# Kernel tuning notes

Measured on AMD Instinct MI355X. Metric: run time of the kernel, lower is better.

Reference implementation:

```python
import jax, jax.numpy as jnp
from jax import lax
import numpy as np

K = 1024      # kernel_size
S = 256       # stride
CUT = 513     # kernel_size//2 + 1
TC = 2 * CUT  # transform_channels = 1026
CH = 8        # combine_hidden
B = 32
TIME = 262144


def setup_inputs() -> dict:
    key = jax.random.key(0)
    ks = jax.random.split(key, 12)
    x = jax.random.normal(ks[0], (B, 1, TIME), dtype=jnp.float32)
    conv1_w = jax.random.normal(ks[1], (TC, 1, K), dtype=jnp.float32) * 0.02
    in_gamma = 1.0 + 0.1 * jax.random.normal(ks[2], (TC,), dtype=jnp.float32)
    comb1_w = jax.random.normal(ks[3], (CH, 2), dtype=jnp.float32) * 0.5
    comb1_b = jax.random.normal(ks[4], (CH,), dtype=jnp.float32) * 0.1
    comb2_w = jax.random.normal(ks[5], (1, CH), dtype=jnp.float32) * 0.5
    comb2_b = jax.random.normal(ks[6], (1,), dtype=jnp.float32) * 0.1
    lin_w = jax.random.normal(ks[7], (CUT, CUT), dtype=jnp.float32) * 0.04
    lin_b = jax.random.normal(ks[8], (CUT,), dtype=jnp.float32) * 0.02
    fc_gamma = 1.0 + 0.1 * jax.random.normal(ks[9], (CUT,), dtype=jnp.float32)
    convT_w = jax.random.normal(ks[10], (TC, 2, K), dtype=jnp.float32) * 0.02  # torch ConvTranspose1d (Cin, Cout, K)
    return {"x": x, "conv1_w": conv1_w, "in_gamma": in_gamma,
            "comb1_w": comb1_w, "comb1_b": comb1_b,
            "comb2_w": comb2_w, "comb2_b": comb2_b,
            "lin_w": lin_w, "lin_b": lin_b, "fc_gamma": fc_gamma,
            "convT_w": convT_w}


def reference(x, conv1_w, in_gamma, comb1_w, comb1_b, comb2_w, comb2_b,
              lin_w, lin_b, fc_gamma, convT_w):
    time = x.shape[2]
    # conv1: Conv1d(1, TC, K, stride=S, padding=K), no bias
    t = lax.conv_general_dilated(x, conv1_w, window_strides=(S,),
                                 padding=[(K, K)],
                                 dimension_numbers=("NCH", "OIH", "NCH"))
    # ConvScaler1d (per-channel scale) + tanh activation
    t = jnp.tanh(t * in_gamma[None, :, None])  # (B, TC, F)
    real_x, imag_x = t[:, :CUT, :], t[:, CUT:, :]
    spec = jnp.stack([real_x, imag_x], axis=1)  # (B, 2, CUT, F)
    # combine1/combine2: 1x1 Conv2d + relu
    h = jax.nn.relu(jnp.einsum("bcxf,oc->boxf", spec, comb1_w)
                    + comb1_b[None, :, None, None])
    h = jax.nn.relu(jnp.einsum("bcxf,oc->boxf", h, comb2_w)
                    + comb2_b[None, :, None, None])[:, 0]  # (B, CUT, F)
    # FC over frequency axis per (batch, frame)
    hh = h.transpose(0, 2, 1)  # (B, F, CUT)
    hh = (hh @ lin_w.T + lin_b) * fc_gamma  # BitwiseLinear + Scaler
    mask = (jnp.tanh(hh) + 1.0) * 0.5       # output_transform -> [0,1]
    mask = mask.transpose(0, 2, 1)          # (B, CUT, F)
    mask = jnp.concatenate([mask, mask], axis=1)  # (B, TC, F)
    t = t * mask
    # conv1_transpose: ConvTranspose1d(TC, 2, K, stride=S), no bias
    wt = jnp.flip(convT_w.transpose(1, 0, 2), axis=2)  # (2, TC, K) flipped
    y = lax.conv_general_dilated(t, wt, window_strides=(1,),
                                 padding=[(K - 1, K - 1)],
                                 lhs_dilation=(S,),
                                 dimension_numbers=("NCH", "OIH", "NCH"))
    y = y[:, :, K:time + K]  # (B, 2, time)
    return jax.nn.softmax(y, axis=1)
```

## Files before the change

### kernel.cpp

```cpp
#include <hip/hip_runtime.h>
#include <cstddef>
#include <cstdint>

#define TIME_N 262144
#define BATCH  32
#define KW     1024
#define ST     256
#define CUTN   513
#define TCN    1026
#define FN     1029
#define FPAD   1152
#define CPAD   1152
#define XLEN   (FPAD * ST + KW)
#define XBLK   (XLEN / 256)

#define MROWS  (BATCH * FN)
#define MP     33024
#define KPH    544
#define NPH    640
#define TBP    1040
#define FLATB  (FN * TBP)
#define KPC    4160

#define PB_XPAD  (XBLK * BATCH)
#define PB_WBF   (PB_XPAD + CPAD)
#define PB_WLIN  (PB_WBF + NPH)
#define PB_TOTAL (PB_WLIN + KPC)

typedef __bf16 bf16x8 __attribute__((ext_vector_type(8)));
typedef float floatx4 __attribute__((ext_vector_type(4)));

__device__ __forceinline__ unsigned short f2bf(float f) {
    union { float f; unsigned u; } v; v.f = f;
    unsigned r = (v.u + 0x7fffu + ((v.u >> 16) & 1u)) >> 16;
    return (unsigned short)r;
}
__device__ __forceinline__ float bf2f(unsigned short s) {
    union { unsigned u; float f; } v; v.u = ((unsigned)s) << 16;
    return v.f;
}
__device__ __forceinline__ int permch(int n) {
    return (n & 1) ? (CUTN + (n >> 1)) : (n >> 1);
}

__device__ __forceinline__ void load_lds16(const void* g, void* l) {
    __builtin_amdgcn_global_load_lds(
        (const __attribute__((address_space(1))) void*)g,
        (__attribute__((address_space(3))) void*)l, 16, 0, 0);
}

__global__ __launch_bounds__(256) void k_prep(
    const float* __restrict__ x, const float* __restrict__ c1w,
    const float* __restrict__ lw, const float* __restrict__ wct,
    unsigned short* __restrict__ xb, unsigned short* __restrict__ wbf,
    unsigned short* __restrict__ wlb, unsigned short* __restrict__ wdb)
{
    const int bid = blockIdx.x;
    if (bid < PB_XPAD) {
        const int b = bid / XBLK;
        const int p = (bid - b * XBLK) * 256 + threadIdx.x;
        const int g = p - KW;
        float v = (g >= 0 && g < TIME_N) ? x[(size_t)b * TIME_N + g] : 0.0f;
        xb[(size_t)b * XLEN + p] = f2bf(v);
    } else if (bid < PB_WBF) {
        const int n = bid - PB_XPAD;
        const int ch = (n < TCN) ? permch(n) : 0;
        for (int k = threadIdx.x; k < KW; k += 256) {
            float v = (n < TCN) ? c1w[(size_t)ch * KW + k] : 0.0f;
            wbf[(size_t)n * KW + k] = f2bf(v);
        }
    } else if (bid < PB_WLIN) {
        const int n = bid - PB_WBF;
        for (int k = threadIdx.x; k < KPH; k += 256) {
            float v = (n < CUTN && k < CUTN) ? lw[(size_t)n * CUTN + k] : 0.0f;
            wlb[(size_t)n * KPH + k] = f2bf(v);
        }
    } else {
        const int k = bid - PB_WLIN;
        const int r = threadIdx.x;
        const int j = k / TBP;
        const int n = k - j * TBP;
        float v = 0.0f;
        if (n < TCN) {
            const int ch = permch(n);
            const int widx = (3 - j) * 256 + r;
            v = wct[(size_t)(2 * ch) * KW + widx] -
                wct[(size_t)(2 * ch + 1) * KW + widx];
        }
        wdb[(size_t)r * KPC + k] = f2bf(v);
    }
}

__global__ __launch_bounds__(256) void k_conv1m(
    const unsigned short* __restrict__ xb, const unsigned short* __restrict__ wb,
    const float* __restrict__ gamma,
    const float* __restrict__ c1w, const float* __restrict__ c1b,
    const float* __restrict__ c2w, const float* __restrict__ c2b,
    unsigned short* __restrict__ tb2, unsigned short* __restrict__ h)
{
    __shared__ __align__(16) unsigned short As[128 * 64];
    __shared__ __align__(16) unsigned short Bs[128 * 64];

    const int b = blockIdx.x, fb = blockIdx.y, cb = blockIdx.z;
    const int f0 = fb * 128, c0 = cb * 128;
    const int tid = threadIdx.x;

    const unsigned short* xrow = xb + (size_t)b * XLEN;
    const unsigned short* ga[4];
    const unsigned short* gb[4];
    int qa[4];
#pragma unroll
    for (int i = 0; i < 4; ++i) {
        const int c = i * 256 + tid;
        const int row = c >> 3;
        const int colb = (c & 7) * 16;
        const int es = (colb ^ ((row & 7) << 4)) >> 1;
        qa[i] = c * 16;
        ga[i] = xrow + (size_t)(f0 + row) * ST + es;
        gb[i] = wb + (size_t)(c0 + row) * KW + es;
    }

    const int wave = tid >> 6, lane = tid & 63;
    const int lm = lane & 15, lq = lane >> 4;
    const int mw = (wave & 1) * 64, nw = (wave >> 1) * 64;
    const int swz = (lm & 7) << 4;
    int abo[2], bbo[2];
#pragma unroll
    for (int ks = 0; ks < 2; ++ks) {
        abo[ks] = (mw + lm) * 128 + ((ks * 64 + lq * 16) ^ swz);
        bbo[ks] = (nw + lm) * 128 + ((ks * 64 + lq * 16) ^ swz);
    }

    floatx4 acc[4][4];
#pragma unroll
    for (int i = 0; i < 4; ++i)
#pragma unroll
        for (int j = 0; j < 4; ++j) acc[i][j] = (floatx4)0.0f;

    const char* Ab = (const char*)As;
    const char* Bb = (const char*)Bs;

    for (int t = 0; t < KW / 64; ++t) {
#pragma unroll
        for (int i = 0; i < 4; ++i) {
            load_lds16(ga[i], (char*)As + qa[i]);
            load_lds16(gb[i], (char*)Bs + qa[i]);
            ga[i] += 64; gb[i] += 64;
        }
        __syncthreads();

        bf16x8 afr[4][2], bfr[4][2];
#pragma unroll
        for (int mt = 0; mt < 4; ++mt)
#pragma unroll
            for (int ks = 0; ks < 2; ++ks)
                afr[mt][ks] = *(const bf16x8*)(Ab + abo[ks] + mt * 2048);
#pragma unroll
        for (int nt = 0; nt < 4; ++nt)
#pragma unroll
            for (int ks = 0; ks < 2; ++ks)
                bfr[nt][ks] = *(const bf16x8*)(Bb + bbo[ks] + nt * 2048);
#pragma unroll
        for (int mt = 0; mt < 4; ++mt)
#pragma unroll
            for (int nt = 0; nt < 4; ++nt)
#pragma unroll
                for (int ks = 0; ks < 2; ++ks)
                    acc[mt][nt] = __builtin_amdgcn_mfma_f32_16x16x32_bf16(
                        afr[mt][ks], bfr[nt][ks], acc[mt][nt], 0, 0, 0);
        __syncthreads();
    }

    float w1[16], b1[8], w2[8];
#pragma unroll
    for (int o = 0; o < 8; ++o) {
        w1[2 * o]     = c1w[2 * o];
        w1[2 * o + 1] = c1w[2 * o + 1];
        b1[o] = c1b[o];
        w2[o] = c2w[o];
    }
    const float b2v = c2b[0];

    unsigned short* tbb = tb2 + (size_t)b * FLATB;
    const bool evenlane = ((lane & 1) == 0);
#pragma unroll
    for (int nt = 0; nt < 4; ++nt) {
        const int n = c0 + nw + nt * 16 + lm;
        const bool valid_c = (n < TCN);
        const float gv = valid_c ? gamma[permch(n)] : 0.0f;
        const int nbase = n & ~1;
        const int ybase = n >> 1;
        const bool store_c = (nbase < TBP);
#pragma unroll
        for (int mt = 0; mt < 4; ++mt) {
#pragma unroll
            for (int rp = 0; rp < 2; ++rp) {
                const int ra = rp * 2;
                const int fa = f0 + mw + mt * 16 + lq * 4 + ra;
                const float ua = acc[mt][nt][ra] * gv;
                const float ub = acc[mt][nt][ra + 1] * gv;
                const float ta  = 2.0f / (1.0f + __expf(-2.0f * ua)) - 1.0f;
                const float tbv = 2.0f / (1.0f + __expf(-2.0f * ub)) - 1.0f;
                const float sa = __shfl_xor(ta, 1);
                const float sb = __shfl_xor(tbv, 1);
                const int  fme = evenlane ? fa : (fa + 1);
                const float re = evenlane ? ta : sb;
                const float im = evenlane ? sa : tbv;
                if (fme < FN) {
                    if (store_c) {
                        const unsigned pr = (unsigned)f2bf(re) |
                                            ((unsigned)f2bf(im) << 16);
                        *(unsigned*)&tbb[(size_t)fme * TBP + nbase] = pr;
                    }
                    if (valid_c) {
                        float a2 = b2v;
#pragma unroll
                        for (int o = 0; o < 8; ++o) {
                            const float a1 = fmaxf(
                                re * w1[2 * o] + im * w1[2 * o + 1] + b1[o], 0.0f);
                            a2 += a1 * w2[o];
                        }
                        h[((size_t)b * FN + fme) * KPH + ybase] =
                            f2bf(fmaxf(a2, 0.0f));
                    }
                }
            }
        }
    }
}

__global__ __launch_bounds__(256) void k_maskm(
    const unsigned short* __restrict__ h, const unsigned short* __restrict__ wlb,
    const float* __restrict__ linb, const float* __restrict__ fcg,
    unsigned* __restrict__ tbu)
{
    __shared__ __align__(16) unsigned short As[128 * 32];
    __shared__ __align__(16) unsigned short Bs[128 * 32];

    const int m0 = blockIdx.x * 128, n0 = blockIdx.y * 128;
    const int tid = threadIdx.x;

    const int s0 = tid, s1 = tid + 256;
    const int ar0 = s0 >> 2, aq0 = s0 & 3;
    const int ar1 = s1 >> 2, aq1 = s1 & 3;
    const unsigned short* ga0 = h + (size_t)(m0 + ar0) * KPH + aq0 * 8;
    const unsigned short* ga1 = h + (size_t)(m0 + ar1) * KPH + aq1 * 8;
    const unsigned short* gb0 = wlb + (size_t)(n0 + ar0) * KPH + aq0 * 8;
    const unsigned short* gb1 = wlb + (size_t)(n0 + ar1) * KPH + aq1 * 8;
    unsigned short* la0 = &As[s0 * 8];
    unsigned short* la1 = &As[s1 * 8];
    unsigned short* lb0 = &Bs[s0 * 8];
    unsigned short* lb1 = &Bs[s1 * 8];

    const int wave = tid >> 6, lane = tid & 63;
    const int lm = lane & 15, lq = lane >> 4;
    const int mw = (wave & 1) * 64, nw = (wave >> 1) * 64;
    const unsigned short* Ap = &As[(mw + lm) * 32 + lq * 8];
    const unsigned short* Bp = &Bs[(nw + lm) * 32 + lq * 8];

    floatx4 acc[4][4];
#pragma unroll
    for (int i = 0; i < 4; ++i)
#pragma unroll
        for (int j = 0; j < 4; ++j) acc[i][j] = (floatx4)0.0f;

    for (int ks = 0; ks < KPH / 32; ++ks) {
        load_lds16(ga0, la0);
        load_lds16(ga1, la1);
        load_lds16(gb0, lb0);
        load_lds16(gb1, lb1);
        ga0 += 32; ga1 += 32; gb0 += 32; gb1 += 32;
        __syncthreads();

        bf16x8 afr[4], bfr[4];
#pragma unroll
        for (int mt = 0; mt < 4; ++mt) afr[mt] = *(const bf16x8*)(Ap + mt * 16 * 32);
#pragma unroll
        for (int nt = 0; nt < 4; ++nt) bfr[nt] = *(const bf16x8*)(Bp + nt * 16 * 32);
#pragma unroll
        for (int mt = 0; mt < 4; ++mt)
#pragma unroll
            for (int nt = 0; nt < 4; ++nt)
                acc[mt][nt] = __builtin_amdgcn_mfma_f32_16x16x32_bf16(
                    afr[mt], bfr[nt], acc[mt][nt], 0, 0, 0);
        __syncthreads();
    }

#pragma unroll
    for (int nt = 0; nt < 4; ++nt) {
        const int y = n0 + nw + nt * 16 + lm;
        if (y < CUTN) {
            const float lb = linb[y];
            const float gv = fcg[y];
#pragma unroll
            for (int mt = 0; mt < 4; ++mt) {
#pragma unroll
                for (int r = 0; r < 4; ++r) {
                    const int m = m0 + mw + mt * 16 + lq * 4 + r;
                    if (m < MROWS) {
                        const float v = (acc[mt][nt][r] + lb) * gv;
                        const float msk = 1.0f / (1.0f + __expf(-2.0f * v));
                        unsigned* p = tbu + (size_t)m * (TBP / 2) + y;
                        const unsigned u = *p;
                        const float re = bf2f((unsigned short)(u & 0xffffu)) * msk;
                        const float im = bf2f((unsigned short)(u >> 16)) * msk;
                        *p = (unsigned)f2bf(re) | ((unsigned)f2bf(im) << 16);
                    }
                }
            }
        }
    }
}

__global__ __launch_bounds__(256) void k_convtm(
    const unsigned short* __restrict__ tb2, const unsigned short* __restrict__ wdb,
    float* __restrict__ out)
{
    __shared__ __align__(16) unsigned short As[128 * 64];
    __shared__ __align__(16) unsigned short Bs[128 * 64];

    const int m0 = blockIdx.x * 128, n0 = blockIdx.y * 128;
    const int b   = m0 >> 10;
    const int ml0 = m0 & 1023;
    const int tid = threadIdx.x;

    const unsigned short* tbb = tb2 + (size_t)b * FLATB;
    const unsigned short* ga[4];
    const unsigned short* gb[4];
    int qa[4];
#pragma unroll
    for (int i = 0; i < 4; ++i) {
        const int c = i * 256 + tid;
        const int row = c >> 3;
        const int colb = (c & 7) * 16;
        const int es = (colb ^ ((row & 7) << 4)) >> 1;
        qa[i] = c * 16;
        ga[i] = tbb + (size_t)(ml0 + row + 1) * TBP + es;
        gb[i] = wdb + (size_t)(n0 + row) * KPC + es;
    }

    const int wave = tid >> 6, lane = tid & 63;
    const int lm = lane & 15, lq = lane >> 4;
    const int mw = (wave & 1) * 64, nw = (wave >> 1) * 64;
    const int swz = (lm & 7) << 4;
    int abo[2], bbo[2];
#pragma unroll
    for (int ks = 0; ks < 2; ++ks) {
        abo[ks] = (mw + lm) * 128 + ((ks * 64 + lq * 16) ^ swz);
        bbo[ks] = (nw + lm) * 128 + ((ks * 64 + lq * 16) ^ swz);
    }

    floatx4 acc[4][4];
#pragma unroll
    for (int i = 0; i < 4; ++i)
#pragma unroll
        for (int j = 0; j < 4; ++j) acc[i][j] = (floatx4)0.0f;

    const char* Ab = (const char*)As;
    const char* Bb = (const char*)Bs;

    for (int t = 0; t < KPC / 64; ++t) {
#pragma unroll
        for (int i = 0; i < 4; ++i) {
            load_lds16(ga[i], (char*)As + qa[i]);
            load_lds16(gb[i], (char*)Bs + qa[i]);
            ga[i] += 64; gb[i] += 64;
        }
        __syncthreads();

        bf16x8 afr[4][2], bfr[4][2];
#pragma unroll
        for (int mt = 0; mt < 4; ++mt)
#pragma unroll
            for (int ks = 0; ks < 2; ++ks)
                afr[mt][ks] = *(const bf16x8*)(Ab + abo[ks] + mt * 2048);
#pragma unroll
        for (int nt = 0; nt < 4; ++nt)
#pragma unroll
            for (int ks = 0; ks < 2; ++ks)
                bfr[nt][ks] = *(const bf16x8*)(Bb + bbo[ks] + nt * 2048);
#pragma unroll
        for (int mt = 0; mt < 4; ++mt)
#pragma unroll
            for (int nt = 0; nt < 4; ++nt)
#pragma unroll
                for (int ks = 0; ks < 2; ++ks)
                    acc[mt][nt] = __builtin_amdgcn_mfma_f32_16x16x32_bf16(
                        afr[mt][ks], bfr[nt][ks], acc[mt][nt], 0, 0, 0);
        __syncthreads();
    }

    float* ob = out + (size_t)b * 2 * TIME_N;
#pragma unroll
    for (int nt = 0; nt < 4; ++nt) {
        const int n = n0 + nw + nt * 16 + lm;
#pragma unroll
        for (int mt = 0; mt < 4; ++mt) {
#pragma unroll
            for (int r = 0; r < 4; ++r) {
                const int m = ml0 + mw + mt * 16 + lq * 4 + r;
                const float d = acc[mt][nt][r];
                const float p0 = 1.0f / (1.0f + __expf(-d));
                const int tau = m * 256 + n;
                ob[tau]          = p0;
                ob[TIME_N + tau] = 1.0f - p0;
            }
        }
    }
}

extern "C" void kernel_launch(void* const* d_in, const int* in_sizes, int n_in,
                              void* d_out, int out_size, void* d_ws, size_t ws_size,
                              hipStream_t stream)
{
    const float* x    = (const float*)d_in[0];
    const float* c1w  = (const float*)d_in[1];
    const float* ing  = (const float*)d_in[2];
    const float* cb1w = (const float*)d_in[3];
    const float* cb1b = (const float*)d_in[4];
    const float* cb2w = (const float*)d_in[5];
    const float* cb2b = (const float*)d_in[6];
    const float* linw = (const float*)d_in[7];
    const float* linb = (const float*)d_in[8];
    const float* fcg  = (const float*)d_in[9];
    const float* ctw  = (const float*)d_in[10];
    float* out = (float*)d_out;

    unsigned short* tb2 = (unsigned short*)d_ws;
    unsigned short* h   = tb2 + (size_t)BATCH * FLATB;
    unsigned short* wlb = h + (size_t)MP * KPH;
    unsigned short* xb  = wlb + (size_t)NPH * KPH;
    unsigned short* wbf = xb + (size_t)BATCH * XLEN;
    unsigned short* wdb = wbf + (size_t)CPAD * KW;

    hipLaunchKernelGGL(k_prep, dim3(PB_TOTAL), dim3(256), 0, stream,
                       x, c1w, linw, ctw, xb, wbf, wlb, wdb);
    hipLaunchKernelGGL(k_conv1m, dim3(BATCH, 9, 9), dim3(256), 0, stream,
                       xb, wbf, ing, cb1w, cb1b, cb2w, cb2b, tb2, h);
    hipLaunchKernelGGL(k_maskm, dim3(MP / 128, NPH / 128), dim3(256), 0, stream,
                       h, wlb, linb, fcg, (unsigned*)tb2);
    hipLaunchKernelGGL(k_convtm, dim3(256, 2), dim3(256), 0, stream,
                       tb2, wdb, out);
}
```

Before: 471.3 us.

## Double-buffer LDS tiles in conv1 and convT GEMM kernels

New measurement: 446.3 us. -5.3%, faster.

```diff
diff --git a/kernel.cpp b/kernel.cpp
--- a/kernel.cpp
+++ b/kernel.cpp
@@ -98,8 +98,7 @@
     const float* __restrict__ c2w, const float* __restrict__ c2b,
     unsigned short* __restrict__ tb2, unsigned short* __restrict__ h)
 {
-    __shared__ __align__(16) unsigned short As[128 * 64];
-    __shared__ __align__(16) unsigned short Bs[128 * 64];
+    extern __shared__ __align__(16) char lds[];
 
     const int b = blockIdx.x, fb = blockIdx.y, cb = blockIdx.z;
     const int f0 = fb * 128, c0 = cb * 128;
@@ -128,7 +127,7 @@
 #pragma unroll
     for (int ks = 0; ks < 2; ++ks) {
         abo[ks] = (mw + lm) * 128 + ((ks * 64 + lq * 16) ^ swz);
-        bbo[ks] = (nw + lm) * 128 + ((ks * 64 + lq * 16) ^ swz);
+        bbo[ks] = 16384 + (nw + lm) * 128 + ((ks * 64 + lq * 16) ^ swz);
     }
 
     floatx4 acc[4][4];
@@ -137,29 +136,38 @@
 #pragma unroll
         for (int j = 0; j < 4; ++j) acc[i][j] = (floatx4)0.0f;
 
-    const char* Ab = (const char*)As;
-    const char* Bb = (const char*)Bs;
+#pragma unroll
+    for (int i = 0; i < 4; ++i) {
+        load_lds16(ga[i], lds + qa[i]);
+        load_lds16(gb[i], lds + 16384 + qa[i]);
+        ga[i] += 64; gb[i] += 64;
+    }
+    __syncthreads();
 
     for (int t = 0; t < KW / 64; ++t) {
-#pragma unroll
-        for (int i = 0; i < 4; ++i) {
-            load_lds16(ga[i], (char*)As + qa[i]);
-            load_lds16(gb[i], (char*)Bs + qa[i]);
-            ga[i] += 64; gb[i] += 64;
-        }
-        __syncthreads();
+        char* cur = lds + (t & 1) * 32768;
+        char* nxt = lds + ((t + 1) & 1) * 32768;
+
+        if (t + 1 < KW / 64) {
+#pragma unroll
+            for (int i = 0; i < 4; ++i) {
+                load_lds16(ga[i], nxt + qa[i]);
+                load_lds16(gb[i], nxt + 16384 + qa[i]);
+                ga[i] += 64; gb[i] += 64;
+            }
+        }
 
         bf16x8 afr[4][2], bfr[4][2];
 #pragma unroll
         for (int mt = 0; mt < 4; ++mt)
 #pragma unroll
             for (int ks = 0; ks < 2; ++ks)
-                afr[mt][ks] = *(const bf16x8*)(Ab + abo[ks] + mt * 2048);
+                afr[mt][ks] = *(const bf16x8*)(cur + abo[ks] + mt * 2048);
 #pragma unroll
         for (int nt = 0; nt < 4; ++nt)
 #pragma unroll
             for (int ks = 0; ks < 2; ++ks)
-                bfr[nt][ks] = *(const bf16x8*)(Bb + bbo[ks] + nt * 2048);
+                bfr[nt][ks] = *(const bf16x8*)(cur + bbo[ks] + nt * 2048);
 #pragma unroll
         for (int mt = 0; mt < 4; ++mt)
 #pragma unroll
@@ -316,8 +324,7 @@
     const unsigned short* __restrict__ tb2, const unsigned short* __restrict__ wdb,
     float* __restrict__ out)
 {
-    __shared__ __align__(16) unsigned short As[128 * 64];
-    __shared__ __align__(16) unsigned short Bs[128 * 64];
+    extern __shared__ __align__(16) char lds[];
 
     const int m0 = blockIdx.x * 128, n0 = blockIdx.y * 128;
     const int b   = m0 >> 10;
@@ -347,7 +354,7 @@
 #pragma unroll
     for (int ks = 0; ks < 2; ++ks) {
         abo[ks] = (mw + lm) * 128 + ((ks * 64 + lq * 16) ^ swz);
-        bbo[ks] = (nw + lm) * 128 + ((ks * 64 + lq * 16) ^ swz);
+        bbo[ks] = 16384 + (nw + lm) * 128 + ((ks * 64 + lq * 16) ^ swz);
     }
 
     floatx4 acc[4][4];
@@ -356,29 +363,38 @@
 #pragma unroll
         for (int j = 0; j < 4; ++j) acc[i][j] = (floatx4)0.0f;
 
-    const char* Ab = (const char*)As;
-    const char* Bb = (const char*)Bs;
+#pragma unroll
+    for (int i = 0; i < 4; ++i) {
+        load_lds16(ga[i], lds + qa[i]);
+        load_lds16(gb[i], lds + 16384 + qa[i]);
+        ga[i] += 64; gb[i] += 64;
+    }
+    __syncthreads();
 
     for (int t = 0; t < KPC / 64; ++t) {
-#pragma unroll
-        for (int i = 0; i < 4; ++i) {
-            load_lds16(ga[i], (char*)As + qa[i]);
-            load_lds16(gb[i], (char*)Bs + qa[i]);
-            ga[i] += 64; gb[i] += 64;
-        }
-        __syncthreads();
+        char* cur = lds + (t & 1) * 32768;
+        char* nxt = lds + ((t + 1) & 1) * 32768;
+
+        if (t + 1 < KPC / 64) {
+#pragma unroll
+            for (int i = 0; i < 4; ++i) {
+                load_lds16(ga[i], nxt + qa[i]);
+                load_lds16(gb[i], nxt + 16384 + qa[i]);
+                ga[i] += 64; gb[i] += 64;
+            }
+        }
 
         bf16x8 afr[4][2], bfr[4][2];
 #pragma unroll
         for (int mt = 0; mt < 4; ++mt)
 #pragma unroll
             for (int ks = 0; ks < 2; ++ks)
-                afr[mt][ks] = *(const bf16x8*)(Ab + abo[ks] + mt * 2048);
+                afr[mt][ks] = *(const bf16x8*)(cur + abo[ks] + mt * 2048);
 #pragma unroll
         for (int nt = 0; nt < 4; ++nt)
 #pragma unroll
             for (int ks = 0; ks < 2; ++ks)
-                bfr[nt][ks] = *(const bf16x8*)(Bb + bbo[ks] + nt * 2048);
+                bfr[nt][ks] = *(const bf16x8*)(cur + bbo[ks] + nt * 2048);
 #pragma unroll
         for (int mt = 0; mt < 4; ++mt)
 #pragma unroll
@@ -435,10 +451,10 @@
 
     hipLaunchKernelGGL(k_prep, dim3(PB_TOTAL), dim3(256), 0, stream,
                        x, c1w, linw, ctw, xb, wbf, wlb, wdb);
-    hipLaunchKernelGGL(k_conv1m, dim3(BATCH, 9, 9), dim3(256), 0, stream,
+    hipLaunchKernelGGL(k_conv1m, dim3(BATCH, 9, 9), dim3(256), 65536, stream,
                        xb, wbf, ing, cb1w, cb1b, cb2w, cb2b, tb2, h);
     hipLaunchKernelGGL(k_maskm, dim3(MP / 128, NPH / 128), dim3(256), 0, stream,
                        h, wlb, linb, fcg, (unsigned*)tb2);
-    hipLaunchKernelGGL(k_convtm, dim3(256, 2), dim3(256), 0, stream,
+    hipLaunchKernelGGL(k_convtm, dim3(256, 2), dim3(256), 65536, stream,
                        tb2, wdb, out);
 }
```
